# Kernel optimization log

Hardware: AMD Instinct MI355X
Metric: run time of the kernel (lower is better)

## Reference

```python
import jax, jax.numpy as jnp
import numpy as np

B = 4096      # number of queries
N = 65536     # number of reference points

def setup_inputs() -> dict:
    key = jax.random.key(0)
    k1, k2, k3 = jax.random.split(key, 3)
    x = jax.random.normal(k1, (B,), dtype=jnp.float32)
    input_tensor = jax.random.normal(k2, (N,), dtype=jnp.float32)
    accuracy_tensor = jax.random.uniform(k3, (N,), dtype=jnp.float32)
    return {"x": x, "input_tensor": input_tensor, "accuracy_tensor": accuracy_tensor}

def reference(x, input_tensor, accuracy_tensor):
    # (B, N) broadcast abs-difference distance matrix
    distances = jnp.abs(input_tensor[None, :] - x[:, None])
    # nearest reference point per query
    min_idx = jnp.argmin(distances, axis=1)          # (B,)
    return accuracy_tensor[min_idx]                  # (B,)
```

## Files before the change

kernel.cpp:

```cpp
#include <hip/hip_runtime.h>

#define CHUNK 512
#define GRP   32
#define QB    4

__global__ __launch_bounds__(256, 8)
void nn_init_kernel(unsigned long long* __restrict__ best, int B) {
    int i = blockIdx.x * 256 + threadIdx.x;
    if (i < B) best[i] = ~0ULL;
}

__global__ __launch_bounds__(256, 8)
void nn_main_kernel(const float* __restrict__ x,
                    const float* __restrict__ pts,
                    unsigned long long* __restrict__ best,
                    int qw_shift)
{
    const int lane = threadIdx.x & 63;
    const int wv = __builtin_amdgcn_readfirstlane((int)(threadIdx.x >> 6));
    const int w  = blockIdx.x * 4 + wv;
    const int qw = w & ((1 << qw_shift) - 1);
    const int ck = w >> qw_shift;

    const int q = (qw << 6) + lane;
    const float xq = x[q];

    const float* __restrict__ pc = pts + (size_t)(unsigned)ck * CHUNK;

    const float inf = __builtin_inff();
    float bdA = inf, bdB = inf, prev = inf;
    int grp = 0;

    #pragma unroll 2
    for (int g = 0; g < CHUNK / GRP; ++g) {
        #pragma unroll
        for (int t = 0; t < GRP / 4; ++t) {
            float p0 = pc[g * GRP + 4 * t + 0];
            float p1 = pc[g * GRP + 4 * t + 1];
            float p2 = pc[g * GRP + 4 * t + 2];
            float p3 = pc[g * GRP + 4 * t + 3];
            bdA = fminf(fminf(fabsf(p0 - xq), fabsf(p1 - xq)), bdA);
            bdB = fminf(fminf(fabsf(p2 - xq), fabsf(p3 - xq)), bdB);
        }
        float cur = fminf(bdA, bdB);
        grp  = (cur < prev) ? g : grp;
        prev = cur;
    }

    const float bd = prev;

    const float4* __restrict__ pg =
        reinterpret_cast<const float4*>(pc + grp * GRP);
    int bi = 0;
    #pragma unroll
    for (int t = GRP / 4 - 1; t >= 0; --t) {
        float4 v = pg[t];
        bi = (fabsf(v.w - xq) == bd) ? 4 * t + 3 : bi;
        bi = (fabsf(v.z - xq) == bd) ? 4 * t + 2 : bi;
        bi = (fabsf(v.y - xq) == bd) ? 4 * t + 1 : bi;
        bi = (fabsf(v.x - xq) == bd) ? 4 * t + 0 : bi;
    }

    const unsigned gidx = (unsigned)(ck * CHUNK + grp * GRP + bi);
    const unsigned long long key =
        ((unsigned long long)__float_as_uint(bd) << 32) | gidx;
    atomicMin(&best[q], key);
}

__global__ __launch_bounds__(256, 8)
void nn_gather_kernel(const unsigned long long* __restrict__ best,
                      const float* __restrict__ acc,
                      float* __restrict__ out, int B) {
    int i = blockIdx.x * 256 + threadIdx.x;
    if (i < B) out[i] = acc[(unsigned)(best[i] & 0xffffffffULL)];
}

__global__ __launch_bounds__(256, 4)
void nn_kernel(const float* __restrict__ x,
               const float* __restrict__ pts,
               const float* __restrict__ acc,
               float* __restrict__ out,
               int B, int N) {
    const int lane = threadIdx.x & 63;
    const int wave = threadIdx.x >> 6;
    const int q    = blockIdx.x * QB + wave;
    if (q >= B) return;

    const float xq = x[q];
    const int G = N >> 2;
    const int J = G >> 6;

    float bd0 = __builtin_inff(), bd1 = __builtin_inff(),
          bd2 = __builtin_inff(), bd3 = __builtin_inff();
    int   bj0 = 0, bj1 = 0, bj2 = 0, bj3 = 0;

    const float4* __restrict__ p4 = reinterpret_cast<const float4*>(pts);

    #pragma unroll 4
    for (int j = 0; j < J; ++j) {
        float4 v = p4[lane + 64 * j];
        float d0 = fabsf(v.x - xq);
        float d1 = fabsf(v.y - xq);
        float d2 = fabsf(v.z - xq);
        float d3 = fabsf(v.w - xq);
        if (d0 < bd0) { bd0 = d0; bj0 = j; }
        if (d1 < bd1) { bd1 = d1; bj1 = j; }
        if (d2 < bd2) { bd2 = d2; bj2 = j; }
        if (d3 < bd3) { bd3 = d3; bj3 = j; }
    }

    unsigned long long key;
    {
        unsigned i0 = (unsigned)(4 * (lane + 64 * bj0) + 0);
        unsigned i1 = (unsigned)(4 * (lane + 64 * bj1) + 1);
        unsigned i2 = (unsigned)(4 * (lane + 64 * bj2) + 2);
        unsigned i3 = (unsigned)(4 * (lane + 64 * bj3) + 3);
        unsigned long long k0 = ((unsigned long long)__float_as_uint(bd0) << 32) | i0;
        unsigned long long k1 = ((unsigned long long)__float_as_uint(bd1) << 32) | i1;
        unsigned long long k2 = ((unsigned long long)__float_as_uint(bd2) << 32) | i2;
        unsigned long long k3 = ((unsigned long long)__float_as_uint(bd3) << 32) | i3;
        key = k0 < k1 ? k0 : k1;
        unsigned long long k23 = k2 < k3 ? k2 : k3;
        key = key < k23 ? key : k23;
    }

    for (int i = J * 256 + lane; i < N; i += 64) {
        float d = fabsf(pts[i] - xq);
        unsigned long long k = ((unsigned long long)__float_as_uint(d) << 32) | (unsigned)i;
        key = key < k ? key : k;
    }

    #pragma unroll
    for (int off = 1; off < 64; off <<= 1) {
        unsigned long long o = __shfl_xor(key, off, 64);
        key = key < o ? key : o;
    }

    if (lane == 0) {
        out[q] = acc[(unsigned)(key & 0xffffffffULL)];
    }
}

extern "C" void kernel_launch(void* const* d_in, const int* in_sizes, int n_in,
                              void* d_out, int out_size, void* d_ws, size_t ws_size,
                              hipStream_t stream) {
    const float* x   = (const float*)d_in[0];
    const float* pts = (const float*)d_in[1];
    const float* acc = (const float*)d_in[2];
    float* out = (float*)d_out;
    const int B = in_sizes[0];
    const int N = in_sizes[1];

    const int nqw = B >> 6;
    const int nchunk = N / CHUNK;
    const bool pow2 = (nqw > 0) && ((nqw & (nqw - 1)) == 0);
    const bool fast = pow2 && (B % 64 == 0) && (N % CHUNK == 0) &&
                      d_ws != nullptr && ws_size >= (size_t)B * 8;

    if (fast) {
        int qw_shift = 0;
        while ((1 << qw_shift) < nqw) ++qw_shift;
        unsigned long long* best = (unsigned long long*)d_ws;

        hipLaunchKernelGGL(nn_init_kernel, dim3((B + 255) / 256), dim3(256), 0,
                           stream, best, B);
        hipLaunchKernelGGL(nn_main_kernel, dim3((nchunk * nqw) / 4), dim3(256),
                           0, stream, x, pts, best, qw_shift);
        hipLaunchKernelGGL(nn_gather_kernel, dim3((B + 255) / 256), dim3(256),
                           0, stream, best, acc, out, B);
    } else {
        const int blocks = (B + QB - 1) / QB;
        hipLaunchKernelGGL(nn_kernel, dim3(blocks), dim3(256), 0, stream,
                           x, pts, acc, out, B, N);
    }
}
```

Baseline: 73.45 us.

## Fuse init/main/gather into one kernel with last-block partial reduction

Replaces the three-kernel pipeline (init, per-chunk atomicMin, gather) with a single kernel. Each block writes its per-chunk best key to a partials buffer, and the last block per query group, found through an atomic counter, reduces across chunks and gathers the accuracy value. The chunk size doubles so there are half as many partials, at the cost of a memset launch, extra global traffic for the partials, and a serial reduction loop over chunks in the last block.

```diff
diff --git a/kernel.cpp b/kernel.cpp
--- a/kernel.cpp
+++ b/kernel.cpp
@@ -1,28 +1,25 @@
 #include <hip/hip_runtime.h>
 
-#define CHUNK 512
+#define CHUNK 1024
 #define GRP   32
 #define QB    4
 
 __global__ __launch_bounds__(256, 8)
-void nn_init_kernel(unsigned long long* __restrict__ best, int B) {
-    int i = blockIdx.x * 256 + threadIdx.x;
-    if (i < B) best[i] = ~0ULL;
-}
+void nn_fused_kernel(const float* __restrict__ x,
+                     const float* __restrict__ pts,
+                     const float* __restrict__ acc,
+                     float* __restrict__ out,
+                     unsigned long long* __restrict__ part,
+                     unsigned int* __restrict__ counters,
+                     int B, int nchunk, int qg_shift)
+{
+    const int tid  = threadIdx.x;
+    const int lane = tid & 63;
+    const int wv   = __builtin_amdgcn_readfirstlane(tid >> 6);
+    const int qg   = blockIdx.x & ((1 << qg_shift) - 1);
+    const int ck   = blockIdx.x >> qg_shift;
 
-__global__ __launch_bounds__(256, 8)
-void nn_main_kernel(const float* __restrict__ x,
-                    const float* __restrict__ pts,
-                    unsigned long long* __restrict__ best,
-                    int qw_shift)
-{
-    const int lane = threadIdx.x & 63;
-    const int wv = __builtin_amdgcn_readfirstlane((int)(threadIdx.x >> 6));
-    const int w  = blockIdx.x * 4 + wv;
-    const int qw = w & ((1 << qw_shift) - 1);
-    const int ck = w >> qw_shift;
-
-    const int q = (qw << 6) + lane;
+    const int q = (qg << 8) + (wv << 6) + lane;
     const float xq = x[q];
 
     const float* __restrict__ pc = pts + (size_t)(unsigned)ck * CHUNK;
@@ -64,15 +61,27 @@
     const unsigned gidx = (unsigned)(ck * CHUNK + grp * GRP + bi);
     const unsigned long long key =
         ((unsigned long long)__float_as_uint(bd) << 32) | gidx;
-    atomicMin(&best[q], key);
-}
 
-__global__ __launch_bounds__(256, 8)
-void nn_gather_kernel(const unsigned long long* __restrict__ best,
-                      const float* __restrict__ acc,
-                      float* __restrict__ out, int B) {
-    int i = blockIdx.x * 256 + threadIdx.x;
-    if (i < B) out[i] = acc[(unsigned)(best[i] & 0xffffffffULL)];
+    part[(size_t)ck * B + q] = key;
+
+    __threadfence();
+    __shared__ int last_flag;
+    if (tid == 0) {
+        unsigned int old = atomicAdd(&counters[qg], 1u);
+        last_flag = (old == (unsigned)(nchunk - 1)) ? 1 : 0;
+    }
+    __syncthreads();
+    if (last_flag) {
+        __threadfence();
+        const int qq = (qg << 8) + tid;
+        unsigned long long bk = ~0ULL;
+        #pragma unroll 8
+        for (int c = 0; c < nchunk; ++c) {
+            unsigned long long k = part[(size_t)c * B + qq];
+            bk = k < bk ? k : bk;
+        }
+        out[qq] = acc[(unsigned)(bk & 0xffffffffULL)];
+    }
 }
 
 __global__ __launch_bounds__(256, 4)
@@ -151,23 +160,27 @@
     const int B = in_sizes[0];
     const int N = in_sizes[1];
 
-    const int nqw = B >> 6;
     const int nchunk = N / CHUNK;
-    const bool pow2 = (nqw > 0) && ((nqw & (nqw - 1)) == 0);
-    const bool fast = pow2 && (B % 64 == 0) && (N % CHUNK == 0) &&
-                      d_ws != nullptr && ws_size >= (size_t)B * 8;
+    const int nqg    = B >> 8;
+    const bool pow2  = (nqg > 0) && ((nqg & (nqg - 1)) == 0);
+
+    const size_t part_bytes = (size_t)nchunk * (size_t)B * 8;
+    const size_t need       = part_bytes + 256 + (size_t)nqg * 4;
+    const bool fast = pow2 && (B % 256 == 0) && (N % CHUNK == 0) &&
+                      d_ws != nullptr && ws_size >= need;
 
     if (fast) {
-        int qw_shift = 0;
-        while ((1 << qw_shift) < nqw) ++qw_shift;
-        unsigned long long* best = (unsigned long long*)d_ws;
+        int qg_shift = 0;
+        while ((1 << qg_shift) < nqg) ++qg_shift;
 
-        hipLaunchKernelGGL(nn_init_kernel, dim3((B + 255) / 256), dim3(256), 0,
-                           stream, best, B);
-        hipLaunchKernelGGL(nn_main_kernel, dim3((nchunk * nqw) / 4), dim3(256),
-                           0, stream, x, pts, best, qw_shift);
-        hipLaunchKernelGGL(nn_gather_kernel, dim3((B + 255) / 256), dim3(256),
-                           0, stream, best, acc, out, B);
+        unsigned long long* part = (unsigned long long*)d_ws;
+        unsigned int* counters =
+            (unsigned int*)((char*)d_ws + ((part_bytes + 255) & ~(size_t)255));
+
+        hipMemsetAsync(counters, 0, (size_t)nqg * 4, stream);
+        hipLaunchKernelGGL(nn_fused_kernel, dim3(nchunk * nqg), dim3(256), 0,
+                           stream, x, pts, acc, out, part, counters,
+                           B, nchunk, qg_shift);
     } else {
         const int blocks = (B + QB - 1) / QB;
         hipLaunchKernelGGL(nn_kernel, dim3(blocks), dim3(256), 0, stream,
```

Result: slower. 149.0 us (+102.9%).
